# Performance work log

Hardware: AMD Instinct MI355X
Metric: run time of the kernel (lower is better)

Reference implementation:

```python
import jax, jax.numpy as jnp
import numpy as np

B, L, I, H, C, E = 32, 2048, 512, 512, 512, 512
TEMP = 0.5
EPS = 1e-20


def setup_inputs() -> dict:
    key = jax.random.key(0)
    ks = jax.random.split(key, 8)
    s_in = 1.0 / np.sqrt(I)
    s_h = 1.0 / np.sqrt(H)
    s_c = 1.0 / np.sqrt(C)
    return {
        "inputs_BxLxI": jax.random.normal(ks[0], (B, L, I), dtype=jnp.float32),
        "W_h": jax.random.uniform(ks[1], (H, I), jnp.float32, -s_in, s_in),
        "b_h": jax.random.uniform(ks[2], (H,), jnp.float32, -s_in, s_in),
        "W_logits": jax.random.uniform(ks[3], (C, H), jnp.float32, -s_h, s_h),
        "b_logits": jax.random.uniform(ks[4], (C,), jnp.float32, -s_h, s_h),
        "codebook_CxE": jax.random.uniform(ks[5], (C, E), jnp.float32, -s_c, s_c),
        "u_noise": jax.random.uniform(ks[6], (B, L, C), dtype=jnp.float32),
        "testing": 0,
    }


def reference(inputs_BxLxI, W_h, b_h, W_logits, b_logits, codebook_CxE, u_noise, testing):
    # 1-layer MLP before quantization
    hiddens = jax.nn.relu(jnp.einsum('bli,hi->blh', inputs_BxLxI, W_h) + b_h)
    logits_BxLxC = jnp.einsum('blh,ch->blc', hiddens, W_logits) + b_logits

    if testing:
        ind = jnp.argmax(logits_BxLxC, axis=-1)
        onehot_BxLxC = jax.nn.one_hot(ind, C, dtype=logits_BxLxC.dtype)
    else:
        # gumbel-softmax with straight-through one-hot
        g = -jnp.log(-jnp.log(u_noise + EPS) + EPS)
        y = jax.nn.softmax((logits_BxLxC + g) / TEMP, axis=-1)
        ind = jnp.argmax(y, axis=-1)
        y_hard = jax.nn.one_hot(ind, C, dtype=y.dtype)
        onehot_BxLxC = jax.lax.stop_gradient(y_hard - y) + y

    # disguised embedding gather: onehot @ codebook
    codes_BxLxE = jnp.einsum('blc,ce->ble', onehot_BxLxC, codebook_CxE)
    return (logits_BxLxC, codes_BxLxE)
```

## Files before the change

### kernel.cpp

```cpp
#include <hip/hip_runtime.h>
#include <hip/hip_fp16.h>

typedef _Float16 h16;
typedef __attribute__((ext_vector_type(8))) _Float16 h16x8;
typedef __attribute__((ext_vector_type(4))) _Float16 h16x4;
typedef __attribute__((ext_vector_type(4))) float f32x4;

#define KDIM 512
#define NDIM 512
#define LO_SCALE 4096.0f
#define LO_INV   0.000244140625f

__device__ __forceinline__ void gload16(const void* g, void* l) {
  __builtin_amdgcn_global_load_lds((const __attribute__((address_space(1))) void*)g,
                                   (__attribute__((address_space(3))) void*)l, 16, 0, 0);
}

#define WAITV(n) asm volatile("s_waitcnt vmcnt(" #n ")" ::: "memory")
#define WAITL0() asm volatile("s_waitcnt lgkmcnt(0)" ::: "memory")
#define SB() __builtin_amdgcn_sched_barrier(0)

__global__ void split_w(const float* __restrict__ Wh, const float* __restrict__ Wl,
                        h16* __restrict__ WhHi, h16* __restrict__ WhLo,
                        h16* __restrict__ WlHi, h16* __restrict__ WlLo) {
  int i = blockIdx.x * 256 + threadIdx.x;
  float a = Wh[i];
  h16 h = (h16)a;
  WhHi[i] = h; WhLo[i] = (h16)((a - (float)h) * LO_SCALE);
  a = Wl[i];
  h = (h16)a;
  WlHi[i] = h; WlLo[i] = (h16)((a - (float)h) * LO_SCALE);
}

__launch_bounds__(256, 2)
__global__ void gemm5_k(const float* __restrict__ X,
                        const h16* __restrict__ BHi, const h16* __restrict__ BLo,
                        const float* __restrict__ bias,
                        h16* __restrict__ OHi, h16* __restrict__ OLo) {
  __shared__ __align__(16) char lds[65536];
  const int tid = threadIdx.x;
  const int wave = tid >> 6, lane = tid & 63;
  const int wg = (blockIdx.x & 7) * 256 + (blockIdx.x >> 3);
  const int bm = wg >> 2, bn = wg & 3;
  const int wm = wave >> 1, wn = wave & 1;
  const long arow0 = (long)bm * 128;
  const int brow0 = bn * 128;
  const int q = lane >> 4, rlo = lane & 15;

  f32x4 acc_hh[4][4] = {};
  f32x4 acc_mx[4][4] = {};
  f32x4 areg[2][4];

  auto aload = [&](f32x4 (&ar)[4], int kt) {
#pragma unroll
    for (int i = 0; i < 4; ++i) {
      int so = i * 4096 + tid * 16;
      int r = so >> 7, cbyte = so & 127;
      ar[i] = *(const f32x4*)((const char*)X + (arow0 + r) * 2048 + (long)kt * 128 + cbyte);
    }
  };
  auto awrite = [&](f32x4 (&ar)[4], int bufoff) {
#pragma unroll
    for (int i = 0; i < 4; ++i) {
      int so = i * 4096 + tid * 16;
      int r = so >> 7;
      int jb = (tid & 7) * 8;
      int sw = ((r & 1) << 6) | (((r >> 1) & 3) << 4);
      f32x4 a = ar[i];
      h16x4 hv, lv;
#pragma unroll
      for (int e = 0; e < 4; ++e) {
        h16 h = (h16)a[e];
        hv[e] = h;
        lv[e] = (h16)((a[e] - (float)h) * LO_SCALE);
      }
      *(h16x4*)(lds + bufoff + r * 128 + (jb ^ sw)) = hv;
      *(h16x4*)(lds + bufoff + r * 128 + ((jb + 64) ^ sw)) = lv;
    }
  };
  auto bgld = [&](int bufoff, int kt) {
#pragma unroll
    for (int pass = 0; pass < 4; ++pass) {
      int p = pass * 4096 + wave * 1024 + lane * 16;
      int row = p >> 7;
      int gs = ((p >> 4) & 7) ^ (row & 7);
      const char* sp = (gs & 4) ? (const char*)BLo : (const char*)BHi;
      long off = (long)(brow0 + row) * 1024 + (long)kt * 64 + (gs & 3) * 16;
      gload16(sp + off, lds + bufoff + 16384 + pass * 4096 + wave * 1024);
    }
  };

  aload(areg[0], 0);
  aload(areg[1], 1);
  WAITV(4);
  awrite(areg[0], 0);
  bgld(0, 0);
  WAITV(4);
  awrite(areg[1], 32768);
  aload(areg[0], 2);
  bgld(32768, 1);
  WAITL0();

#pragma unroll
  for (int t = 0; t < 16; ++t) {
    if (t <= 13) { WAITV(8); } else if (t == 14) { WAITV(4); } else { WAITV(0); }
    SB();
    __builtin_amdgcn_s_barrier();
    SB();

    if (t <= 12) aload(areg[(t + 3) & 1], t + 3);

    const char* buf = lds + (t & 1) * 32768;
    h16x8 ah[4], al[4], bh[4], bl[4];
#pragma unroll
    for (int i = 0; i < 4; ++i) {
      int row = wm * 64 + i * 16 + rlo;
      int swa = ((row & 1) << 6) | (((row >> 1) & 3) << 4);
      ah[i] = *(const h16x8*)(buf + row * 128 + ((q * 16) ^ swa));
      al[i] = *(const h16x8*)(buf + row * 128 + ((q * 16 + 64) ^ swa));
      int rb = wn * 64 + i * 16 + rlo;
      int swb = (rb & 7) << 4;
      bh[i] = *(const h16x8*)(buf + 16384 + rb * 128 + ((q * 16) ^ swb));
      bl[i] = *(const h16x8*)(buf + 16384 + rb * 128 + ((q * 16 + 64) ^ swb));
    }
#pragma unroll
    for (int i = 0; i < 4; ++i)
#pragma unroll
      for (int j = 0; j < 4; ++j)
        acc_hh[i][j] = __builtin_amdgcn_mfma_f32_16x16x32_f16(ah[i], bh[j], acc_hh[i][j], 0, 0, 0);
#pragma unroll
    for (int i = 0; i < 4; ++i)
#pragma unroll
      for (int j = 0; j < 4; ++j)
        acc_mx[i][j] = __builtin_amdgcn_mfma_f32_16x16x32_f16(ah[i], bl[j], acc_mx[i][j], 0, 0, 0);
#pragma unroll
    for (int i = 0; i < 4; ++i)
#pragma unroll
      for (int j = 0; j < 4; ++j)
        acc_mx[i][j] = __builtin_amdgcn_mfma_f32_16x16x32_f16(al[i], bh[j], acc_mx[i][j], 0, 0, 0);

    WAITL0();
    SB();
    __builtin_amdgcn_s_barrier();
    SB();
    if (t <= 12) {
      WAITV(8);
      awrite(areg[(t + 2) & 1], (t & 1) * 32768);
      bgld((t & 1) * 32768, t + 2);
    } else if (t == 13) {
      WAITV(4);
      awrite(areg[1], 32768);
      bgld(32768, 15);
    }
  }

#pragma unroll
  for (int j = 0; j < 4; ++j) {
    int lcol = wn * 64 + j * 16 + rlo;
    float bv = bias[bn * 128 + lcol];
#pragma unroll
    for (int i = 0; i < 4; ++i)
#pragma unroll
      for (int r = 0; r < 4; ++r) {
        int lrow = wm * 64 + i * 16 + q * 4 + r;
        float v = fmaxf(acc_hh[i][j][r] + acc_mx[i][j][r] * LO_INV + bv, 0.0f);
        h16 h = (h16)v;
        h16 l = (h16)((v - (float)h) * LO_SCALE);
        unsigned uu = (unsigned)__builtin_bit_cast(unsigned short, h) |
                      ((unsigned)__builtin_bit_cast(unsigned short, l) << 16);
        *(unsigned*)(lds + lrow * 512 + lcol * 4) = uu;
      }
  }
  __syncthreads();
#pragma unroll
  for (int pass = 0; pass < 16; ++pass) {
    int o = pass * 4096 + tid * 16;
    int lrow = o >> 9;
    int lcb = o & 511;
    uint4 d = *(const uint4*)(lds + o);
    uint2 hi, lo;
    hi.x = (d.x & 0xffffu) | (d.y << 16);
    hi.y = (d.z & 0xffffu) | (d.w << 16);
    lo.x = (d.x >> 16) | (d.y & 0xffff0000u);
    lo.y = (d.z >> 16) | (d.w & 0xffff0000u);
    long gb = (arow0 + lrow) * 1024 + bn * 256 + (lcb >> 1);
    *(uint2*)((char*)OHi + gb) = hi;
    *(uint2*)((char*)OLo + gb) = lo;
  }
}

template <int AF32, int EPI>
__launch_bounds__(256, 2)
__global__ void gemm4_k(const void* __restrict__ Aptr, const void* __restrict__ AptrLo,
                        const h16* __restrict__ BHi, const h16* __restrict__ BLo,
                        const float* __restrict__ bias,
                        float* __restrict__ Cf32,
                        h16* __restrict__ OHi, h16* __restrict__ OLo) {
  __shared__ __align__(16) char lds[65536];
  const int tid = threadIdx.x;
  const int wave = tid >> 6, lane = tid & 63;
  const int wg = (blockIdx.x & 7) * 256 + (blockIdx.x >> 3);
  const int bm = wg >> 2, bn = wg & 3;
  const int wm = wave >> 1, wn = wave & 1;
  const long arow0 = (long)bm * 128;
  const int brow0 = bn * 128;
  const int q = lane >> 4, rlo = lane & 15;

  f32x4 acc_hh[4][4] = {};
  f32x4 acc_mx[4][4] = {};

#define STAGE4(bufoff, kt)                                                    \
  {                                                                           \
    _Pragma("unroll")                                                         \
    for (int pass = 0; pass < 4; ++pass) {                                    \
      int p = pass * 4096 + wave * 1024 + lane * 16;                          \
      int row = p >> 7;                                                       \
      int gs = ((p >> 4) & 7) ^ (row & 7);                                    \
      const char* sp = (gs & 4) ? (const char*)AptrLo : (const char*)Aptr;    \
      long off = (arow0 + row) * 1024 + (kt) * 64 + (gs & 3) * 16;            \
      gload16(sp + off, lds + (bufoff) + pass * 4096 + wave * 1024);          \
    }                                                                         \
    _Pragma("unroll")                                                         \
    for (int pass = 0; pass < 4; ++pass) {                                    \
      int p = pass * 4096 + wave * 1024 + lane * 16;                          \
      int row = p >> 7;                                                       \
      int gs = ((p >> 4) & 7) ^ (row & 7);                                    \
      const char* sp = (gs & 4) ? (const char*)BLo : (const char*)BHi;        \
      long off = (long)(brow0 + row) * 1024 + (kt) * 64 + (gs & 3) * 16;      \
      gload16(sp + off, lds + (bufoff) + 16384 + pass * 4096 + wave * 1024);  \
    }                                                                         \
  }

  STAGE4(0, 0);
  STAGE4(32768, 1);

#pragma unroll
  for (int t = 0; t < 16; ++t) {
    if (t < 15) { WAITV(8); } else { WAITV(0); }
    SB();
    __builtin_amdgcn_s_barrier();
    SB();

    const char* buf = lds + (t & 1) * 32768;
    h16x8 ah[4], al[4], bh[4], bl[4];
#pragma unroll
    for (int i = 0; i < 4; ++i) {
      int row = wm * 64 + i * 16 + rlo;
      int sw = (row & 7) << 4;
      ah[i] = *(const h16x8*)(buf + row * 128 + ((q * 16) ^ sw));
      al[i] = *(const h16x8*)(buf + row * 128 + ((q * 16 + 64) ^ sw));
      int rb = wn * 64 + i * 16 + rlo;
      int swb = (rb & 7) << 4;
      bh[i] = *(const h16x8*)(buf + 16384 + rb * 128 + ((q * 16) ^ swb));
      bl[i] = *(const h16x8*)(buf + 16384 + rb * 128 + ((q * 16 + 64) ^ swb));
    }
#pragma unroll
    for (int i = 0; i < 4; ++i)
#pragma unroll
      for (int j = 0; j < 4; ++j)
        acc_hh[i][j] = __builtin_amdgcn_mfma_f32_16x16x32_f16(ah[i], bh[j], acc_hh[i][j], 0, 0, 0);
#pragma unroll
    for (int i = 0; i < 4; ++i)
#pragma unroll
      for (int j = 0; j < 4; ++j)
        acc_mx[i][j] = __builtin_amdgcn_mfma_f32_16x16x32_f16(ah[i], bl[j], acc_mx[i][j], 0, 0, 0);
#pragma unroll
    for (int i = 0; i < 4; ++i)
#pragma unroll
      for (int j = 0; j < 4; ++j)
        acc_mx[i][j] = __builtin_amdgcn_mfma_f32_16x16x32_f16(al[i], bh[j], acc_mx[i][j], 0, 0, 0);

    WAITL0();
    SB();
    __builtin_amdgcn_s_barrier();
    SB();
    if (t + 2 < 16) STAGE4((t & 1) * 32768, t + 2);
  }
#undef STAGE4

#pragma unroll
  for (int j = 0; j < 4; ++j) {
    int lcol = wn * 64 + j * 16 + rlo;
    float bv = bias[bn * 128 + lcol];
#pragma unroll
    for (int i = 0; i < 4; ++i)
#pragma unroll
      for (int r = 0; r < 4; ++r) {
        int lrow = wm * 64 + i * 16 + q * 4 + r;
        float v = acc_hh[i][j][r] + acc_mx[i][j][r] * LO_INV + bv;
        if (EPI == 0) {
          v = fmaxf(v, 0.0f);
          h16 h = (h16)v;
          h16 l = (h16)((v - (float)h) * LO_SCALE);
          unsigned uu = (unsigned)__builtin_bit_cast(unsigned short, h) |
                        ((unsigned)__builtin_bit_cast(unsigned short, l) << 16);
          *(unsigned*)(lds + lrow * 512 + lcol * 4) = uu;
        } else {
          *(float*)(lds + lrow * 512 + lcol * 4) = v;
        }
      }
  }
  __syncthreads();
#pragma unroll
  for (int pass = 0; pass < 16; ++pass) {
    int o = pass * 4096 + tid * 16;
    int lrow = o >> 9;
    int lcb = o & 511;
    if (EPI == 0) {
      uint4 d = *(const uint4*)(lds + o);
      uint2 hi, lo;
      hi.x = (d.x & 0xffffu) | (d.y << 16);
      hi.y = (d.z & 0xffffu) | (d.w << 16);
      lo.x = (d.x >> 16) | (d.y & 0xffff0000u);
      lo.y = (d.z >> 16) | (d.w & 0xffff0000u);
      long gb = (arow0 + lrow) * 1024 + bn * 256 + (lcb >> 1);
      *(uint2*)((char*)OHi + gb) = hi;
      *(uint2*)((char*)OLo + gb) = lo;
    } else {
      f32x4 d = *(const f32x4*)(lds + o);
      long gb = (arow0 + lrow) * 2048 + bn * 512 + lcb;
      *(f32x4*)((char*)Cf32 + gb) = d;
    }
  }
}

__global__ void k3_argmax_gather(const float* __restrict__ logits,
                                 const float* __restrict__ u,
                                 const float* __restrict__ cb,
                                 const int* __restrict__ testing,
                                 float* __restrict__ codes) {
  const int wave = threadIdx.x >> 6, lane = threadIdx.x & 63;
  const long row = (long)blockIdx.x * 4 + wave;
  const f32x4* lrow = (const f32x4*)(logits + row * 512);
  const f32x4* urow = (const f32x4*)(u + row * 512);
  const int test = *testing;

  float best = -3.4e38f;
  int bi = 0;
#pragma unroll
  for (int h = 0; h < 2; ++h) {
    int c4 = h * 64 + lane;
    f32x4 z = lrow[c4];
    if (!test) {
      f32x4 uu = urow[c4];
#pragma unroll
      for (int t = 0; t < 4; ++t)
        z[t] += -logf(-logf(uu[t] + 1e-20f) + 1e-20f);
    }
#pragma unroll
    for (int t = 0; t < 4; ++t) {
      int c = c4 * 4 + t;
      if (z[t] > best) { best = z[t]; bi = c; }
    }
  }
#pragma unroll
  for (int off = 32; off; off >>= 1) {
    float ob = __shfl_xor(best, off);
    int oi = __shfl_xor(bi, off);
    if (ob > best || (ob == best && oi < bi)) { best = ob; bi = oi; }
  }
  const f32x4* src = (const f32x4*)(cb + (long)bi * 512);
  f32x4* dst = (f32x4*)(codes + row * 512);
  dst[lane] = src[lane];
  dst[lane + 64] = src[lane + 64];
}

extern "C" void kernel_launch(void* const* d_in, const int* in_sizes, int n_in,
                              void* d_out, int out_size, void* d_ws, size_t ws_size,
                              hipStream_t stream) {
  const float* X = (const float*)d_in[0];
  const float* Wh = (const float*)d_in[1];
  const float* bh = (const float*)d_in[2];
  const float* Wl = (const float*)d_in[3];
  const float* bl = (const float*)d_in[4];
  const float* cb = (const float*)d_in[5];
  const float* u = (const float*)d_in[6];
  const int* testing = (const int*)d_in[7];

  float* logits = (float*)d_out;
  float* codes = logits + 33554432;
  h16* Hhi = (h16*)codes;
  h16* Hlo = Hhi + 33554432;

  h16* WhHi = (h16*)d_ws;
  h16* WhLo = WhHi + 262144;
  h16* WlHi = WhLo + 262144;
  h16* WlLo = WlHi + 262144;

  split_w<<<dim3(1024), dim3(256), 0, stream>>>(Wh, Wl, WhHi, WhLo, WlHi, WlLo);

  gemm5_k<<<dim3(2048), dim3(256), 0, stream>>>(X, WhHi, WhLo, bh, Hhi, Hlo);

  gemm4_k<0, 1><<<dim3(2048), dim3(256), 0, stream>>>(
      (const void*)Hhi, (const void*)Hlo, WlHi, WlLo, bl, logits, nullptr, nullptr);

  k3_argmax_gather<<<dim3(16384), dim3(256), 0, stream>>>(logits, u, cb, testing, codes);
}
```

Baseline: 301.9 us.

## Retile first GEMM to full-width 64x512 blocks so X is read once

Replaces the 128x128-tile first GEMM with a 512-thread kernel that computes a 64-row by full 512-column tile. The fp32 input rows are loaded and split into hi/lo halves once per row instead of once per column block, which cuts redundant global reads and conversion work. The B tile is now the whole weight slab, so LDS use grows to about 144KB per block. That likely limits occupancy to one block per CU and makes latency hiding rely on the 8 waves. The second GEMM's template parameters and argument types are also simplified, with no speed intent.

```diff
diff --git a/kernel.cpp b/kernel.cpp
--- a/kernel.cpp
+++ b/kernel.cpp
@@ -32,96 +32,85 @@
   WlHi[i] = h; WlLo[i] = (h16)((a - (float)h) * LO_SCALE);
 }
 
-__launch_bounds__(256, 2)
-__global__ void gemm5_k(const float* __restrict__ X,
+__launch_bounds__(512, 2)
+__global__ void gemm6_k(const float* __restrict__ X,
                         const h16* __restrict__ BHi, const h16* __restrict__ BLo,
                         const float* __restrict__ bias,
                         h16* __restrict__ OHi, h16* __restrict__ OLo) {
-  __shared__ __align__(16) char lds[65536];
+  __shared__ __align__(16) char lds[147456];
   const int tid = threadIdx.x;
   const int wave = tid >> 6, lane = tid & 63;
-  const int wg = (blockIdx.x & 7) * 256 + (blockIdx.x >> 3);
-  const int bm = wg >> 2, bn = wg & 3;
-  const int wm = wave >> 1, wn = wave & 1;
-  const long arow0 = (long)bm * 128;
-  const int brow0 = bn * 128;
+  const int wn = wave;
+  const long arow0 = (long)blockIdx.x * 64;
   const int q = lane >> 4, rlo = lane & 15;
 
   f32x4 acc_hh[4][4] = {};
   f32x4 acc_mx[4][4] = {};
-  f32x4 areg[2][4];
-
-  auto aload = [&](f32x4 (&ar)[4], int kt) {
-#pragma unroll
-    for (int i = 0; i < 4; ++i) {
-      int so = i * 4096 + tid * 16;
-      int r = so >> 7, cbyte = so & 127;
-      ar[i] = *(const f32x4*)((const char*)X + (arow0 + r) * 2048 + (long)kt * 128 + cbyte);
-    }
+  f32x4 areg[2];
+
+  const int axrow = tid >> 3;
+  const int ajb = (tid & 7) * 8;
+  const int asw = ((axrow & 1) << 6) | (((axrow >> 1) & 3) << 4);
+
+  auto aload = [&](f32x4& ar, int kt) {
+    ar = *(const f32x4*)((const char*)X + (arow0 + axrow) * 2048 +
+                         (long)kt * 128 + (tid & 7) * 16);
   };
-  auto awrite = [&](f32x4 (&ar)[4], int bufoff) {
-#pragma unroll
-    for (int i = 0; i < 4; ++i) {
-      int so = i * 4096 + tid * 16;
-      int r = so >> 7;
-      int jb = (tid & 7) * 8;
-      int sw = ((r & 1) << 6) | (((r >> 1) & 3) << 4);
-      f32x4 a = ar[i];
-      h16x4 hv, lv;
-#pragma unroll
-      for (int e = 0; e < 4; ++e) {
-        h16 h = (h16)a[e];
-        hv[e] = h;
-        lv[e] = (h16)((a[e] - (float)h) * LO_SCALE);
-      }
-      *(h16x4*)(lds + bufoff + r * 128 + (jb ^ sw)) = hv;
-      *(h16x4*)(lds + bufoff + r * 128 + ((jb + 64) ^ sw)) = lv;
-    }
+  auto awrite = [&](const f32x4& ar, char* buf) {
+    h16x4 hv, lv;
+#pragma unroll
+    for (int e = 0; e < 4; ++e) {
+      h16 h = (h16)ar[e];
+      hv[e] = h;
+      lv[e] = (h16)((ar[e] - (float)h) * LO_SCALE);
+    }
+    *(h16x4*)(buf + axrow * 128 + (ajb ^ asw)) = hv;
+    *(h16x4*)(buf + axrow * 128 + ((ajb + 64) ^ asw)) = lv;
   };
-  auto bgld = [&](int bufoff, int kt) {
-#pragma unroll
-    for (int pass = 0; pass < 4; ++pass) {
-      int p = pass * 4096 + wave * 1024 + lane * 16;
+  auto bgld = [&](char* buf, int kt) {
+#pragma unroll
+    for (int pass = 0; pass < 8; ++pass) {
+      int p = pass * 8192 + wave * 1024 + lane * 16;
       int row = p >> 7;
       int gs = ((p >> 4) & 7) ^ (row & 7);
       const char* sp = (gs & 4) ? (const char*)BLo : (const char*)BHi;
-      long off = (long)(brow0 + row) * 1024 + (long)kt * 64 + (gs & 3) * 16;
-      gload16(sp + off, lds + bufoff + 16384 + pass * 4096 + wave * 1024);
+      long off = (long)row * 1024 + (long)kt * 64 + (gs & 3) * 16;
+      gload16(sp + off, buf + 8192 + pass * 8192 + wave * 1024);
     }
   };
 
   aload(areg[0], 0);
   aload(areg[1], 1);
-  WAITV(4);
-  awrite(areg[0], 0);
-  bgld(0, 0);
-  WAITV(4);
-  awrite(areg[1], 32768);
+  WAITV(1);
+  awrite(areg[0], lds);
+  bgld(lds, 0);
+  WAITV(8);
+  awrite(areg[1], lds + 73728);
   aload(areg[0], 2);
-  bgld(32768, 1);
+  bgld(lds + 73728, 1);
   WAITL0();
 
 #pragma unroll
   for (int t = 0; t < 16; ++t) {
-    if (t <= 13) { WAITV(8); } else if (t == 14) { WAITV(4); } else { WAITV(0); }
+    if (t <= 13) { WAITV(9); } else if (t == 14) { WAITV(8); } else { WAITV(0); }
     SB();
     __builtin_amdgcn_s_barrier();
     SB();
 
     if (t <= 12) aload(areg[(t + 3) & 1], t + 3);
 
-    const char* buf = lds + (t & 1) * 32768;
+    char* buf = lds + (t & 1) * 73728;
     h16x8 ah[4], al[4], bh[4], bl[4];
 #pragma unroll
     for (int i = 0; i < 4; ++i) {
-      int row = wm * 64 + i * 16 + rlo;
+      int row = i * 16 + rlo;
       int swa = ((row & 1) << 6) | (((row >> 1) & 3) << 4);
       ah[i] = *(const h16x8*)(buf + row * 128 + ((q * 16) ^ swa));
       al[i] = *(const h16x8*)(buf + row * 128 + ((q * 16 + 64) ^ swa));
       int rb = wn * 64 + i * 16 + rlo;
       int swb = (rb & 7) << 4;
-      bh[i] = *(const h16x8*)(buf + 16384 + rb * 128 + ((q * 16) ^ swb));
-      bl[i] = *(const h16x8*)(buf + 16384 + rb * 128 + ((q * 16 + 64) ^ swb));
+      bh[i] = *(const h16x8*)(buf + 8192 + rb * 128 + ((q * 16) ^ swb));
+      bl[i] = *(const h16x8*)(buf + 8192 + rb * 128 + ((q * 16 + 64) ^ swb));
     }
 #pragma unroll
     for (int i = 0; i < 4; ++i)
@@ -144,54 +133,54 @@
     __builtin_amdgcn_s_barrier();
     SB();
     if (t <= 12) {
+      WAITV(9);
+      awrite(areg[(t + 2) & 1], lds + (t & 1) * 73728);
+      bgld(lds + (t & 1) * 73728, t + 2);
+    } else if (t == 13) {
       WAITV(8);
-      awrite(areg[(t + 2) & 1], (t & 1) * 32768);
-      bgld((t & 1) * 32768, t + 2);
-    } else if (t == 13) {
-      WAITV(4);
-      awrite(areg[1], 32768);
-      bgld(32768, 15);
+      awrite(areg[1], lds + 73728);
+      bgld(lds + 73728, 15);
     }
   }
 
 #pragma unroll
   for (int j = 0; j < 4; ++j) {
     int lcol = wn * 64 + j * 16 + rlo;
-    float bv = bias[bn * 128 + lcol];
+    float bv = bias[lcol];
 #pragma unroll
     for (int i = 0; i < 4; ++i)
 #pragma unroll
       for (int r = 0; r < 4; ++r) {
-        int lrow = wm * 64 + i * 16 + q * 4 + r;
+        int lrow = i * 16 + q * 4 + r;
         float v = fmaxf(acc_hh[i][j][r] + acc_mx[i][j][r] * LO_INV + bv, 0.0f);
         h16 h = (h16)v;
         h16 l = (h16)((v - (float)h) * LO_SCALE);
         unsigned uu = (unsigned)__builtin_bit_cast(unsigned short, h) |
                       ((unsigned)__builtin_bit_cast(unsigned short, l) << 16);
-        *(unsigned*)(lds + lrow * 512 + lcol * 4) = uu;
+        *(unsigned*)(lds + lrow * 2048 + lcol * 4) = uu;
       }
   }
   __syncthreads();
 #pragma unroll
   for (int pass = 0; pass < 16; ++pass) {
-    int o = pass * 4096 + tid * 16;
-    int lrow = o >> 9;
-    int lcb = o & 511;
+    int o = pass * 8192 + tid * 16;
+    int lrow = o >> 11;
+    int lcb = o & 2047;
     uint4 d = *(const uint4*)(lds + o);
     uint2 hi, lo;
     hi.x = (d.x & 0xffffu) | (d.y << 16);
     hi.y = (d.z & 0xffffu) | (d.w << 16);
     lo.x = (d.x >> 16) | (d.y & 0xffff0000u);
     lo.y = (d.z >> 16) | (d.w & 0xffff0000u);
-    long gb = (arow0 + lrow) * 1024 + bn * 256 + (lcb >> 1);
+    long gb = (arow0 + lrow) * 1024 + (lcb >> 1);
     *(uint2*)((char*)OHi + gb) = hi;
     *(uint2*)((char*)OLo + gb) = lo;
   }
 }
 
-template <int AF32, int EPI>
+template <int EPI>
 __launch_bounds__(256, 2)
-__global__ void gemm4_k(const void* __restrict__ Aptr, const void* __restrict__ AptrLo,
+__global__ void gemm4_k(const h16* __restrict__ AHi, const h16* __restrict__ ALo,
                         const h16* __restrict__ BHi, const h16* __restrict__ BLo,
                         const float* __restrict__ bias,
                         float* __restrict__ Cf32,
@@ -216,7 +205,7 @@
       int p = pass * 4096 + wave * 1024 + lane * 16;                          \
       int row = p >> 7;                                                       \
       int gs = ((p >> 4) & 7) ^ (row & 7);                                    \
-      const char* sp = (gs & 4) ? (const char*)AptrLo : (const char*)Aptr;    \
+      const char* sp = (gs & 4) ? (const char*)ALo : (const char*)AHi;        \
       long off = (arow0 + row) * 1024 + (kt) * 64 + (gs & 3) * 16;            \
       gload16(sp + off, lds + (bufoff) + pass * 4096 + wave * 1024);          \
     }                                                                         \
@@ -389,10 +378,10 @@
 
   split_w<<<dim3(1024), dim3(256), 0, stream>>>(Wh, Wl, WhHi, WhLo, WlHi, WlLo);
 
-  gemm5_k<<<dim3(2048), dim3(256), 0, stream>>>(X, WhHi, WhLo, bh, Hhi, Hlo);
-
-  gemm4_k<0, 1><<<dim3(2048), dim3(256), 0, stream>>>(
-      (const void*)Hhi, (const void*)Hlo, WlHi, WlLo, bl, logits, nullptr, nullptr);
+  gemm6_k<<<dim3(1024), dim3(512), 0, stream>>>(X, WhHi, WhLo, bh, Hhi, Hlo);
+
+  gemm4_k<1><<<dim3(2048), dim3(256), 0, stream>>>(Hhi, Hlo, WlHi, WlLo, bl,
+                                                   logits, nullptr, nullptr);
 
   k3_argmax_gather<<<dim3(16384), dim3(256), 0, stream>>>(logits, u, cb, testing, codes);
 }
```

After: 318.2 us. 1.05x slower.
